# Performance work log

Measured on AMD Instinct MI355X. Metric: run time of the kernel, lower is better.

The kernel has to match this reference:

```python
import jax, jax.numpy as jnp
import numpy as np

B, LP, LE, D, H, DK, DV, DF = 16, 2047, 2048, 1024, 16, 64, 64, 4096


def _layer_norm(x, g, b, eps=1e-5):
    m = x.mean(-1, keepdims=True)
    v = ((x - m) ** 2).mean(-1, keepdims=True)
    return (x - m) * jax.lax.rsqrt(v + eps) * g + b


def _mha(q, kv, wq, wk, wv, wo, bo, g, b):
    # q: [B,Q,D], kv: [B,L,D]; per-head projections wq/wk: [H,D,DK], wv: [H,D,DV]
    residual = q
    Q = jnp.einsum('bqd,hdk->bhqk', q, wq)
    K = jnp.einsum('bld,hdk->bhlk', kv, wk)
    V = jnp.einsum('bld,hdv->bhlv', kv, wv)
    scale = jnp.sqrt(jnp.asarray(Q.shape[-1], Q.dtype))
    attn = jax.nn.softmax(jnp.einsum('bhqk,bhlk->bhql', Q, K) / scale, axis=-1)
    o = jnp.einsum('bhql,bhlv->bhqv', attn, V)
    o = o.transpose(0, 2, 1, 3).reshape(q.shape[0], q.shape[1], -1)  # concat heads
    o = o @ wo + bo
    return _layer_norm(o + residual, g, b), attn


def setup_inputs() -> dict:
    key = jax.random.key(0)
    ks = jax.random.split(key, 16)
    s = 0.02
    inp = {
        'dec_input': jax.random.normal(ks[0], (B, 1, D), jnp.float32),
        'input_history': jax.random.normal(ks[1], (B, LP, D), jnp.float32),
        'enc_output': jax.random.normal(ks[2], (B, LE, D), jnp.float32),
        'wq_s': jax.random.normal(ks[3], (H, D, DK), jnp.float32) * s,
        'wk_s': jax.random.normal(ks[4], (H, D, DK), jnp.float32) * s,
        'wv_s': jax.random.normal(ks[5], (H, D, DV), jnp.float32) * s,
        'wo_s': jax.random.normal(ks[6], (H * DV, D), jnp.float32) * s,
        'bo_s': jnp.zeros((D,), jnp.float32),
        'ln1_g': jnp.ones((D,), jnp.float32),
        'ln1_b': jnp.zeros((D,), jnp.float32),
        'wq_c': jax.random.normal(ks[7], (H, D, DK), jnp.float32) * s,
        'wk_c': jax.random.normal(ks[8], (H, D, DK), jnp.float32) * s,
        'wv_c': jax.random.normal(ks[9], (H, D, DV), jnp.float32) * s,
        'wo_c': jax.random.normal(ks[10], (H * DV, D), jnp.float32) * s,
        'bo_c': jnp.zeros((D,), jnp.float32),
        'ln2_g': jnp.ones((D,), jnp.float32),
        'ln2_b': jnp.zeros((D,), jnp.float32),
        'ffn_w1': jax.random.normal(ks[11], (D, DF), jnp.float32) * s,
        'ffn_b1': jnp.zeros((DF,), jnp.float32),
        'ffn_w2': jax.random.normal(ks[12], (DF, D), jnp.float32) * s,
        'ffn_b2': jnp.zeros((D,), jnp.float32),
        'ln3_g': jnp.ones((D,), jnp.float32),
        'ln3_b': jnp.zeros((D,), jnp.float32),
    }
    return inp


def reference(dec_input, input_history, enc_output,
              wq_s, wk_s, wv_s, wo_s, bo_s, ln1_g, ln1_b,
              wq_c, wk_c, wv_c, wo_c, bo_c, ln2_g, ln2_b,
              ffn_w1, ffn_b1, ffn_w2, ffn_b2, ln3_g, ln3_b):
    # KV-cache growth: history <- cat(history, dec_input)
    history = jnp.concatenate([input_history, dec_input], axis=1)  # [B, LP+1, D]
    x, slf_attn = _mha(dec_input, history, wq_s, wk_s, wv_s, wo_s, bo_s, ln1_g, ln1_b)
    x, enc_attn = _mha(x, enc_output, wq_c, wk_c, wv_c, wo_c, bo_c, ln2_g, ln2_b)
    y = jax.nn.relu(x @ ffn_w1 + ffn_b1) @ ffn_w2 + ffn_b2
    out = _layer_norm(y + x, ln3_g, ln3_b)
    return (out, slf_attn, enc_attn)
```

## Files before the change

### kernel.cpp

```cpp
#include <hip/hip_runtime.h>
#include <hip/hip_bf16.h>
#include <stdint.h>
#include <stddef.h>


#define DEV __device__ __forceinline__

typedef __attribute__((ext_vector_type(8))) short bf16x8;
typedef __attribute__((ext_vector_type(4))) short bf16x4;
typedef __attribute__((ext_vector_type(4))) float f32x4;

DEV unsigned short f2b(float f){
  union { __hip_bfloat16 h; unsigned short u; } cv;
  cv.h = __float2bfloat16(f);
  return cv.u;
}
DEV float b2f(unsigned short u){
  union { unsigned int i; float f; } cv;
  cv.i = ((unsigned int)u) << 16;
  return cv.f;
}
DEV f32x4 mfma16(bf16x8 a, bf16x8 b, f32x4 c){
  return __builtin_amdgcn_mfma_f32_16x16x32_bf16(a, b, c, 0, 0, 0);
}

__global__ __launch_bounds__(256) void g_qA(const float* __restrict__ src,
    const float* __restrict__ wq, float* __restrict__ Qpart){
  int ks = blockIdx.x, h = blockIdx.y;
  int k0b = ks*128;
  __shared__ unsigned short lt[2][64*40];
  int t = threadIdx.x, lane = t & 63, w = t >> 6;
  int k_loc = t >> 3, n_off = (t & 7)*8;
  const float* apf = src + (size_t)(lane & 15)*1024 + (lane >> 4)*8 + k0b;
  const float* Wb = wq + (size_t)h*65536;
  f32x4 acc = {0.f,0.f,0.f,0.f};
  float4 x0, x1;
  auto LD = [&](int c){
    const float* wp = Wb + (size_t)(k0b + c*32 + k_loc)*64 + n_off;
    x0 = *(const float4*)wp;
    x1 = *(const float4*)(wp + 4);
  };
  auto ST = [&](int buf){
    unsigned short* p = &lt[buf][0];
    p[(n_off+0)*40 + k_loc] = f2b(x0.x);
    p[(n_off+1)*40 + k_loc] = f2b(x0.y);
    p[(n_off+2)*40 + k_loc] = f2b(x0.z);
    p[(n_off+3)*40 + k_loc] = f2b(x0.w);
    p[(n_off+4)*40 + k_loc] = f2b(x1.x);
    p[(n_off+5)*40 + k_loc] = f2b(x1.y);
    p[(n_off+6)*40 + k_loc] = f2b(x1.z);
    p[(n_off+7)*40 + k_loc] = f2b(x1.w);
  };
  LD(0); ST(0);
  for(int c=0; c<4; ++c){
    if(c+1 < 4) LD(c+1);
    __syncthreads();
    float4 a0 = *(const float4*)(apf + c*32);
    float4 a1 = *(const float4*)(apf + c*32 + 4);
    bf16x8 af;
    af[0]=(short)f2b(a0.x); af[1]=(short)f2b(a0.y);
    af[2]=(short)f2b(a0.z); af[3]=(short)f2b(a0.w);
    af[4]=(short)f2b(a1.x); af[5]=(short)f2b(a1.y);
    af[6]=(short)f2b(a1.z); af[7]=(short)f2b(a1.w);
    bf16x8 bv = *(const bf16x8*)&lt[c&1][(w*16 + (lane & 15))*40 + (lane >> 4)*8];
    acc = mfma16(af, bv, acc);
    if(c+1 < 4) ST((c+1)&1);
  }
  int col = w*16 + (lane & 15);
  int r0 = (lane >> 4)*4;
  #pragma unroll
  for(int i=0;i<4;++i)
    Qpart[ ((size_t)(h*8 + ks)*16 + r0 + i)*64 + col ] = acc[i];
}

__global__ __launch_bounds__(256) void g_qB(const float* __restrict__ wk,
    const float* __restrict__ Qpart, unsigned short* __restrict__ qpb){
  int dt = blockIdx.x, h = blockIdx.y;
  int t = threadIdx.x;
  __shared__ float Qs[1024];
  #pragma unroll
  for(int i=0;i<4;++i){
    int idx = i*256 + t;
    float s = 0.f;
    #pragma unroll
    for(int ks=0; ks<8; ++ks)
      s += Qpart[((size_t)h<<13) + (ks<<10) + idx];
    Qs[idx] = s * 0.125f;
  }
  __syncthreads();
  int d_loc = t & 63, bg = t >> 6;
  const float* wr = wk + (size_t)h*65536 + (size_t)(dt*64 + d_loc)*64;
  float acc[4] = {0.f,0.f,0.f,0.f};
  #pragma unroll
  for(int k4=0; k4<16; ++k4){
    float4 w4 = *(const float4*)(wr + k4*4);
    #pragma unroll
    for(int i=0;i<4;++i){
      const float* q = &Qs[(bg*4+i)*64 + k4*4];
      acc[i] += w4.x*q[0] + w4.y*q[1] + w4.z*q[2] + w4.w*q[3];
    }
  }
  #pragma unroll
  for(int i=0;i<4;++i)
    qpb[ ((size_t)(bg*4+i)*16 + h)*1024 + dt*64 + d_loc ] = f2b(acc[i]);
}

__global__ __launch_bounds__(256) void g_attn(const float* __restrict__ kvsrc,
    const float* __restrict__ decrow, const unsigned short* __restrict__ qpb,
    float* __restrict__ scr, unsigned short* __restrict__ partb,
    float* __restrict__ msum, int lsrc){
  int u = blockIdx.x, ns = u & 63, b = u >> 6;
  int t = threadIdx.x, lane = t & 63, w = t >> 6;
  int r = lane & 15, hi = lane >> 4;
  int slice0 = ns*32;

  __shared__ unsigned short lt[1024*20];
  __shared__ float red[1024];
  __shared__ unsigned short p_lds[16*40];
  __shared__ float f_lds[16];

  float4 ld[16];
  auto ISSUE = [&](int c){
    int row = slice0 + c*16 + r;
    const float* rpp = (row < lsrc) ? kvsrc + ((size_t)b*lsrc + row)*1024
                                    : decrow + (size_t)b*1024;
    rpp += w*256 + hi*8;
    #pragma unroll
    for(int kk=0; kk<8; ++kk){
      ld[kk*2+0] = *(const float4*)(rpp + kk*32);
      ld[kk*2+1] = *(const float4*)(rpp + kk*32 + 4);
    }
  };

  ISSUE(0);
  for(int i=t; i<16*40; i+=256) p_lds[i] = 0;

  bf16x8 qf[8];
  {
    const unsigned short* qp = qpb + ((size_t)b*16 + r)*1024 + w*256 + hi*8;
    #pragma unroll
    for(int kk=0;kk<8;++kk) qf[kk] = *(const bf16x8*)(qp + kk*32);
  }

  f32x4 acc[16];
  #pragma unroll
  for(int i=0;i<16;++i) acc[i] = (f32x4){0.f,0.f,0.f,0.f};
  float m_run = -1e30f, s_run = 0.f;

  __syncthreads();
  for(int c=0; c<2; ++c){
    f32x4 s_acc = {0.f,0.f,0.f,0.f};
    int colw = r ^ ((hi & 1) << 3);
    #pragma unroll
    for(int kk=0; kk<8; ++kk){
      float4 a0 = ld[kk*2], a1 = ld[kk*2+1];
      bf16x8 v;
      v[0]=(short)f2b(a0.x); v[1]=(short)f2b(a0.y);
      v[2]=(short)f2b(a0.z); v[3]=(short)f2b(a0.w);
      v[4]=(short)f2b(a1.x); v[5]=(short)f2b(a1.y);
      v[6]=(short)f2b(a1.z); v[7]=(short)f2b(a1.w);
      unsigned short* pt = &lt[(w*256 + hi*8 + kk*32)*20 + colw];
      #pragma unroll
      for(int j=0;j<8;++j) pt[j*20] = (unsigned short)v[j];
      s_acc = mfma16(v, qf[kk], s_acc);
    }
    if(c < 1) ISSUE(c+1);
    *(f32x4*)&red[t*4] = s_acc;
    __syncthreads();

    f32x4 ss = *(const f32x4*)&red[(0*64+lane)*4];
    ss += *(const f32x4*)&red[(1*64+lane)*4];
    ss += *(const f32x4*)&red[(2*64+lane)*4];
    ss += *(const f32x4*)&red[(3*64+lane)*4];
    float sf[4] = {ss[0], ss[1], ss[2], ss[3]};
    float mc = fmaxf(fmaxf(sf[0],sf[1]), fmaxf(sf[2],sf[3]));
    mc = fmaxf(mc, __shfl_xor(mc, 16));
    mc = fmaxf(mc, __shfl_xor(mc, 32));
    float nm = fmaxf(m_run, mc);
    float fch = __expf(m_run - nm);
    float pvv[4]; float ps = 0.f;
    #pragma unroll
    for(int i=0;i<4;++i){ pvv[i] = __expf(sf[i]-nm); ps += pvv[i]; }
    ps += __shfl_xor(ps, 16);
    ps += __shfl_xor(ps, 32);
    s_run = s_run*fch + ps;
    m_run = nm;
    if(w == 0){
      #pragma unroll
      for(int i=0;i<4;++i) p_lds[r*40 + hi*4 + i] = f2b(pvv[i]);
      if(hi == 0) f_lds[r] = fch;
      float* sp = scr + ((size_t)b*16 + r)*2048 + slice0 + c*16 + hi*4;
      *(float4*)sp = (float4){sf[0], sf[1], sf[2], sf[3]};
    }
    __syncthreads();

    f32x4 fv = *(const f32x4*)&f_lds[hi*4];
    bf16x8 pa = *(const bf16x8*)&p_lds[r*40 + hi*8];
    #pragma unroll
    for(int dc=0; dc<16; ++dc){
      acc[dc] *= fv;
      int d = w*256 + dc*16 + r;
      int col0 = (((hi & 1) ^ ((r >> 3) & 1)) << 3);
      bf16x4 blo = *(const bf16x4*)&lt[d*20 + col0];
      bf16x4 bhi = *(const bf16x4*)&lt[d*20 + col0 + 4];
      bf16x8 bv;
      bv[0]=blo[0]; bv[1]=blo[1]; bv[2]=blo[2]; bv[3]=blo[3];
      bv[4]=bhi[0]; bv[5]=bhi[1]; bv[6]=bhi[2]; bv[7]=bhi[3];
      acc[dc] = mfma16(pa, bv, acc[dc]);
    }
    __syncthreads();
  }
  unsigned short* pl = lt;
  #pragma unroll
  for(int dc=0; dc<16; ++dc)
    #pragma unroll
    for(int i=0;i<4;++i)
      pl[(hi*4+i)*1024 + w*256 + dc*16 + r] = f2b(acc[dc][i]);
  __syncthreads();
  {
    const uint4* s4 = (const uint4*)pl;
    uint4* d4 = (uint4*)(partb + (((size_t)b*64 + ns)*16)*1024);
    #pragma unroll
    for(int j=0;j<8;++j) d4[t + j*256] = s4[t + j*256];
  }
  if(w==0 && hi==0){
    msum[(((size_t)b*64 + ns)*16 + r)*2 + 0] = m_run;
    msum[(((size_t)b*64 + ns)*16 + r)*2 + 1] = s_run;
  }
}

__global__ __launch_bounds__(256) void g_comb(const float* __restrict__ msum,
    const float* __restrict__ scr, const unsigned short* __restrict__ partb,
    float* __restrict__ attn_out, unsigned short* __restrict__ ctxb){
  int dq = blockIdx.x, bh = blockIdx.y, b = bh >> 4, h = bh & 15;
  int t = threadIdx.x;
  __shared__ float e_lds[64];
  __shared__ float Mi[2];
  if(t < 64){
    float2 ms = *(const float2*)&msum[(((size_t)b*64 + t)*16 + h)*2];
    float M = ms.x;
    #pragma unroll
    for(int o=1; o<64; o<<=1) M = fmaxf(M, __shfl_xor(M, o));
    float e = __expf(ms.x - M)*ms.y;
    float S = e;
    #pragma unroll
    for(int o=1; o<64; o<<=1) S += __shfl_xor(S, o);
    e_lds[t] = __expf(ms.x - M)/S;
    if(t == 0){ Mi[0] = M; Mi[1] = 1.f/S; }
  }
  __syncthreads();
  float M = Mi[0], inv = Mi[1];
  const float* sp = scr + (size_t)bh*2048 + dq*512;
  float* po = attn_out + (size_t)bh*2048 + dq*512;
  po[t]     = __expf(sp[t]     - M)*inv;
  po[t+256] = __expf(sp[t+256] - M)*inv;
  int d = dq*256 + t;
  const unsigned short* pb0 = partb + ((size_t)b*64*16 + h)*1024 + d;
  float acc = 0.f;
  #pragma unroll 8
  for(int ns=0; ns<64; ++ns)
    acc += e_lds[ns]*b2f(pb0[(size_t)ns*16384]);
  ctxb[(size_t)bh*1024 + d] = f2b(acc);
}

__global__ __launch_bounds__(256) void g_vproj(const float* __restrict__ wv,
    const unsigned short* __restrict__ ctxb, float* __restrict__ opart){
  int ks = blockIdx.x, h = blockIdx.y;
  int k0b = ks*128;
  __shared__ unsigned short lt[2][64*40];
  int t = threadIdx.x, lane = t & 63, w = t >> 6;
  int k_loc = t >> 3, n_off = (t & 7)*8;
  const unsigned short* apb = ctxb + (size_t)(lane & 15)*16384 + (size_t)h*1024
                              + (lane >> 4)*8 + k0b;
  const float* Wb = wv + (size_t)h*65536;
  f32x4 acc = {0.f,0.f,0.f,0.f};
  float4 x0, x1;
  auto LD = [&](int c){
    const float* wp = Wb + (size_t)(k0b + c*32 + k_loc)*64 + n_off;
    x0 = *(const float4*)wp;
    x1 = *(const float4*)(wp + 4);
  };
  auto ST = [&](int buf){
    unsigned short* p = &lt[buf][0];
    p[(n_off+0)*40 + k_loc] = f2b(x0.x);
    p[(n_off+1)*40 + k_loc] = f2b(x0.y);
    p[(n_off+2)*40 + k_loc] = f2b(x0.z);
    p[(n_off+3)*40 + k_loc] = f2b(x0.w);
    p[(n_off+4)*40 + k_loc] = f2b(x1.x);
    p[(n_off+5)*40 + k_loc] = f2b(x1.y);
    p[(n_off+6)*40 + k_loc] = f2b(x1.z);
    p[(n_off+7)*40 + k_loc] = f2b(x1.w);
  };
  LD(0); ST(0);
  for(int c=0; c<4; ++c){
    if(c+1 < 4) LD(c+1);
    __syncthreads();
    bf16x8 af = *(const bf16x8*)(apb + c*32);
    bf16x8 bv = *(const bf16x8*)&lt[c&1][(w*16 + (lane & 15))*40 + (lane >> 4)*8];
    acc = mfma16(af, bv, acc);
    if(c+1 < 4) ST((c+1)&1);
  }
  int col = w*16 + (lane & 15);
  int r0 = (lane >> 4)*4;
  #pragma unroll
  for(int i=0;i<4;++i)
    opart[ ((size_t)(h*8 + ks)*16 + r0 + i)*64 + col ] = acc[i];
}

__global__ __launch_bounds__(256) void g_ovred(const float* __restrict__ opart,
    unsigned short* __restrict__ ob){
  int i = blockIdx.x*256 + threadIdx.x;
  int b = i >> 10, hv = i & 1023, h = hv >> 6, v = hv & 63;
  float s = 0.f;
  #pragma unroll
  for(int ks=0; ks<8; ++ks)
    s += opart[ ((size_t)(h*8 + ks)*16 + b)*64 + v ];
  ob[(size_t)b*1024 + hv] = f2b(s);
}

__global__ __launch_bounds__(256) void g_ln(const float* __restrict__ parts, int KS,
    const float* __restrict__ bias, const float* __restrict__ resid,
    const float* __restrict__ g, const float* __restrict__ bb,
    float* __restrict__ xout, unsigned short* __restrict__ xb16){
  int b = blockIdx.x, t = threadIdx.x;
  __shared__ float red[256];
  const float4* bias4  = (const float4*)bias;
  const float4* resid4 = (const float4*)resid + (size_t)b*256;
  const float4* parts4 = (const float4*)parts;
  float4 s = bias4[t];
  { float4 rr = resid4[t]; s.x+=rr.x; s.y+=rr.y; s.z+=rr.z; s.w+=rr.w; }
  #pragma unroll 4
  for(int k=0;k<KS;++k){
    float4 pp = parts4[((size_t)k*16 + b)*256 + t];
    s.x+=pp.x; s.y+=pp.y; s.z+=pp.z; s.w+=pp.w;
  }
  red[t] = s.x+s.y+s.z+s.w; __syncthreads();
  for(int off=128; off>0; off>>=1){ if(t<off) red[t]+=red[t+off]; __syncthreads(); }
  float mean = red[0]*(1.f/1024.f); __syncthreads();
  float dx=s.x-mean, dy=s.y-mean, dz=s.z-mean, dw=s.w-mean;
  red[t] = dx*dx+dy*dy+dz*dz+dw*dw; __syncthreads();
  for(int off=128; off>0; off>>=1){ if(t<off) red[t]+=red[t+off]; __syncthreads(); }
  float rstd = rsqrtf(red[0]*(1.f/1024.f) + 1e-5f);
  float4 g4 = ((const float4*)g)[t], b4 = ((const float4*)bb)[t];
  float4 y;
  y.x = dx*rstd*g4.x + b4.x;
  y.y = dy*rstd*g4.y + b4.y;
  y.z = dz*rstd*g4.z + b4.z;
  y.w = dw*rstd*g4.w + b4.w;
  if(xout) ((float4*)xout)[(size_t)b*256 + t] = y;
  if(xb16){
    ushort4 uu;
    uu.x = f2b(y.x); uu.y = f2b(y.y); uu.z = f2b(y.z); uu.w = f2b(y.w);
    ((ushort4*)xb16)[(size_t)b*256 + t] = uu;
  }
}

__global__ __launch_bounds__(256) void g_skg(const float* __restrict__ W,
    const unsigned short* __restrict__ A, float* __restrict__ part,
    int N, int K, int KS){
  int nt = blockIdx.x, ks = blockIdx.y;
  int Ksl = K / KS, k0b = ks * Ksl, n0 = nt*64;
  int nc = Ksl >> 5;
  __shared__ unsigned short lt[2][64*40];
  int t = threadIdx.x, lane = t & 63, w = t >> 6;
  int k_loc = t >> 3, n_off = (t & 7)*8;
  const unsigned short* apb = A + (size_t)(lane & 15)*K + (lane >> 4)*8 + k0b;
  f32x4 acc = {0.f,0.f,0.f,0.f};
  float4 x0, x1;
  auto LD = [&](int c){
    const float* wp = W + (size_t)(k0b + c*32 + k_loc)*N + n0 + n_off;
    x0 = *(const float4*)wp;
    x1 = *(const float4*)(wp + 4);
  };
  auto ST = [&](int buf){
    unsigned short* p = &lt[buf][0];
    p[(n_off+0)*40 + k_loc] = f2b(x0.x);
    p[(n_off+1)*40 + k_loc] = f2b(x0.y);
    p[(n_off+2)*40 + k_loc] = f2b(x0.z);
    p[(n_off+3)*40 + k_loc] = f2b(x0.w);
    p[(n_off+4)*40 + k_loc] = f2b(x1.x);
    p[(n_off+5)*40 + k_loc] = f2b(x1.y);
    p[(n_off+6)*40 + k_loc] = f2b(x1.z);
    p[(n_off+7)*40 + k_loc] = f2b(x1.w);
  };
  LD(0); ST(0);
  for(int c=0; c<nc; ++c){
    if(c+1 < nc) LD(c+1);
    __syncthreads();
    bf16x8 af = *(const bf16x8*)(apb + c*32);
    bf16x8 bv = *(const bf16x8*)&lt[c&1][(w*16 + (lane & 15))*40 + (lane >> 4)*8];
    acc = mfma16(af, bv, acc);
    if(c+1 < nc) ST((c+1)&1);
  }
  int col = n0 + w*16 + (lane & 15);
  int r0 = (lane >> 4)*4;
  #pragma unroll
  for(int i=0;i<4;++i)
    part[ ((size_t)ks*16 + r0 + i)*(size_t)N + col ] = acc[i];
}

__global__ __launch_bounds__(256) void g_relu(const float* __restrict__ parts, int KS,
    const float* __restrict__ b1, unsigned short* __restrict__ h1){
  int i = blockIdx.x*256 + threadIdx.x;
  int b = i >> 10, f4 = i & 1023;
  float4 s = ((const float4*)b1)[f4];
  #pragma unroll 4
  for(int k=0;k<KS;++k){
    float4 pp = ((const float4*)parts)[((size_t)k*16 + b)*1024 + f4];
    s.x+=pp.x; s.y+=pp.y; s.z+=pp.z; s.w+=pp.w;
  }
  ushort4 uu;
  uu.x = f2b(fmaxf(s.x,0.f)); uu.y = f2b(fmaxf(s.y,0.f));
  uu.z = f2b(fmaxf(s.z,0.f)); uu.w = f2b(fmaxf(s.w,0.f));
  ((ushort4*)h1)[i] = uu;
}

extern "C" void kernel_launch(void* const* d_in, const int* in_sizes, int n_in,
                              void* d_out, int out_size, void* d_ws, size_t ws_size,
                              hipStream_t stream){
  const float* dec    = (const float*)d_in[0];
  const float* hist   = (const float*)d_in[1];
  const float* enc    = (const float*)d_in[2];
  const float* wq_s   = (const float*)d_in[3];
  const float* wk_s   = (const float*)d_in[4];
  const float* wv_s   = (const float*)d_in[5];
  const float* wo_s   = (const float*)d_in[6];
  const float* bo_s   = (const float*)d_in[7];
  const float* ln1_g  = (const float*)d_in[8];
  const float* ln1_b  = (const float*)d_in[9];
  const float* wq_c   = (const float*)d_in[10];
  const float* wk_c   = (const float*)d_in[11];
  const float* wv_c   = (const float*)d_in[12];
  const float* wo_c   = (const float*)d_in[13];
  const float* bo_c   = (const float*)d_in[14];
  const float* ln2_g  = (const float*)d_in[15];
  const float* ln2_b  = (const float*)d_in[16];
  const float* w1     = (const float*)d_in[17];
  const float* b1     = (const float*)d_in[18];
  const float* w2     = (const float*)d_in[19];
  const float* b2     = (const float*)d_in[20];
  const float* ln3_g  = (const float*)d_in[21];
  const float* ln3_b  = (const float*)d_in[22];

  float* out  = (float*)d_out;
  float* slf  = out + 16384;
  float* enco = out + 16384 + 524288;

  char* w = (char*)d_ws;
  float*          scr    = (float*)(w + 0x0000000);
  unsigned short* partb  = (unsigned short*)(w + 0x0200000);
  float*          msum   = (float*)(w + 0x2200000);
  unsigned short* qpb    = (unsigned short*)(w + 0x2240000);
  unsigned short* ctxb   = (unsigned short*)(w + 0x22C0000);
  float*          Qpart  = (float*)(w + 0x2340000);
  float*          opart  = (float*)(w + 0x23C0000);
  unsigned short* ob     = (unsigned short*)(w + 0x2440000);
  float*          x1     = (float*)(w + 0x2450000);
  float*          x2     = (float*)(w + 0x2460000);
  unsigned short* x2b    = (unsigned short*)(w + 0x2470000);
  unsigned short* h1b    = (unsigned short*)(w + 0x2480000);
  float*          gpart  = (float*)(w + 0x2500000);
  float*          fpart  = (float*)(w + 0x2600000);
  float*          g2part = (float*)(w + 0x2800000);

  g_qA   <<<dim3(8,16),  256, 0, stream>>>(dec, wq_s, Qpart);
  g_qB   <<<dim3(16,16), 256, 0, stream>>>(wk_s, Qpart, qpb);
  g_attn <<<1024, 256, 0, stream>>>(hist, dec, qpb, scr, partb, msum, 2047);
  g_comb <<<dim3(4,256), 256, 0, stream>>>(msum, scr, partb, slf, ctxb);
  g_vproj<<<dim3(8,16),  256, 0, stream>>>(wv_s, ctxb, opart);
  g_ovred<<<64,   256, 0, stream>>>(opart, ob);
  g_skg  <<<dim3(16,16), 256, 0, stream>>>(wo_s, ob, gpart, 1024, 1024, 16);
  g_ln   <<<16,   256, 0, stream>>>(gpart, 16, bo_s, dec, ln1_g, ln1_b, x1, (unsigned short*)0);

  g_qA   <<<dim3(8,16),  256, 0, stream>>>(x1, wq_c, Qpart);
  g_qB   <<<dim3(16,16), 256, 0, stream>>>(wk_c, Qpart, qpb);
  g_attn <<<1024, 256, 0, stream>>>(enc, dec, qpb, scr, partb, msum, 2048);
  g_comb <<<dim3(4,256), 256, 0, stream>>>(msum, scr, partb, enco, ctxb);
  g_vproj<<<dim3(8,16),  256, 0, stream>>>(wv_c, ctxb, opart);
  g_ovred<<<64,   256, 0, stream>>>(opart, ob);
  g_skg  <<<dim3(16,16), 256, 0, stream>>>(wo_c, ob, gpart, 1024, 1024, 16);
  g_ln   <<<16,   256, 0, stream>>>(gpart, 16, bo_c, x1, ln2_g, ln2_b, x2, x2b);

  g_skg  <<<dim3(64,8),  256, 0, stream>>>(w1, x2b, fpart, 4096, 1024, 8);
  g_relu <<<64,  256, 0, stream>>>(fpart, 8, b1, h1b);
  g_skg  <<<dim3(16,32), 256, 0, stream>>>(w2, h1b, g2part, 1024, 4096, 32);
  g_ln   <<<16,  256, 0, stream>>>(g2part, 32, b2, x2, ln3_g, ln3_b, out, (unsigned short*)0);
}
```

Measured before the change: 166.8 us.

## Fuse Q/K projection, V/O projection and ReLU reduction into fewer kernels

Merges the split-K Q projection and its reduction with the Wk query-folding into one kernel, so the Q partial buffer and one launch go away. It also fuses the V projection, its reduction and the Wo projection into one per-head kernel that writes per-head partials for the layer norm. The ReLU and bias reduction is folded into the A-operand load of the second FFN GEMM. Launch count and intermediate traffic drop, but each fused kernel now recomputes the full-K Q and V projections per block with fewer blocks (4x16), so parallelism falls and work is duplicated.

```diff
diff --git a/kernel.cpp b/kernel.cpp
--- a/kernel.cpp
+++ b/kernel.cpp
@@ -24,19 +24,20 @@
   return __builtin_amdgcn_mfma_f32_16x16x32_bf16(a, b, c, 0, 0, 0);
 }
 
-__global__ __launch_bounds__(256) void g_qA(const float* __restrict__ src,
-    const float* __restrict__ wq, float* __restrict__ Qpart){
-  int ks = blockIdx.x, h = blockIdx.y;
-  int k0b = ks*128;
+__global__ __launch_bounds__(256) void g_qp(const float* __restrict__ src,
+    const float* __restrict__ wq, const float* __restrict__ wk,
+    unsigned short* __restrict__ qpb){
+  int dt = blockIdx.x, h = blockIdx.y;
   __shared__ unsigned short lt[2][64*40];
+  __shared__ float Qs[1024];
   int t = threadIdx.x, lane = t & 63, w = t >> 6;
   int k_loc = t >> 3, n_off = (t & 7)*8;
-  const float* apf = src + (size_t)(lane & 15)*1024 + (lane >> 4)*8 + k0b;
+  const float* apf = src + (size_t)(lane & 15)*1024 + (lane >> 4)*8;
   const float* Wb = wq + (size_t)h*65536;
   f32x4 acc = {0.f,0.f,0.f,0.f};
   float4 x0, x1;
   auto LD = [&](int c){
-    const float* wp = Wb + (size_t)(k0b + c*32 + k_loc)*64 + n_off;
+    const float* wp = Wb + (size_t)(c*32 + k_loc)*64 + n_off;
     x0 = *(const float4*)wp;
     x1 = *(const float4*)(wp + 4);
   };
@@ -52,8 +53,8 @@
     p[(n_off+7)*40 + k_loc] = f2b(x1.w);
   };
   LD(0); ST(0);
-  for(int c=0; c<4; ++c){
-    if(c+1 < 4) LD(c+1);
+  for(int c=0; c<32; ++c){
+    if(c+1 < 32) LD(c+1);
     __syncthreads();
     float4 a0 = *(const float4*)(apf + c*32);
     float4 a1 = *(const float4*)(apf + c*32 + 4);
@@ -64,45 +65,32 @@
     af[6]=(short)f2b(a1.z); af[7]=(short)f2b(a1.w);
     bf16x8 bv = *(const bf16x8*)&lt[c&1][(w*16 + (lane & 15))*40 + (lane >> 4)*8];
     acc = mfma16(af, bv, acc);
-    if(c+1 < 4) ST((c+1)&1);
-  }
-  int col = w*16 + (lane & 15);
-  int r0 = (lane >> 4)*4;
-  #pragma unroll
-  for(int i=0;i<4;++i)
-    Qpart[ ((size_t)(h*8 + ks)*16 + r0 + i)*64 + col ] = acc[i];
-}
-
-__global__ __launch_bounds__(256) void g_qB(const float* __restrict__ wk,
-    const float* __restrict__ Qpart, unsigned short* __restrict__ qpb){
-  int dt = blockIdx.x, h = blockIdx.y;
-  int t = threadIdx.x;
-  __shared__ float Qs[1024];
-  #pragma unroll
-  for(int i=0;i<4;++i){
-    int idx = i*256 + t;
-    float s = 0.f;
-    #pragma unroll
-    for(int ks=0; ks<8; ++ks)
-      s += Qpart[((size_t)h<<13) + (ks<<10) + idx];
-    Qs[idx] = s * 0.125f;
+    if(c+1 < 32) ST((c+1)&1);
+  }
+  {
+    int col = w*16 + (lane & 15);
+    int r0 = (lane >> 4)*4;
+    #pragma unroll
+    for(int i=0;i<4;++i) Qs[(r0+i)*64 + col] = acc[i]*0.125f;
   }
   __syncthreads();
-  int d_loc = t & 63, bg = t >> 6;
-  const float* wr = wk + (size_t)h*65536 + (size_t)(dt*64 + d_loc)*64;
-  float acc[4] = {0.f,0.f,0.f,0.f};
+  int d = dt*256 + t;
+  const float* wr = wk + (size_t)h*65536 + (size_t)d*64;
+  float a16[16];
+  #pragma unroll
+  for(int b=0;b<16;++b) a16[b] = 0.f;
   #pragma unroll
   for(int k4=0; k4<16; ++k4){
     float4 w4 = *(const float4*)(wr + k4*4);
     #pragma unroll
-    for(int i=0;i<4;++i){
-      const float* q = &Qs[(bg*4+i)*64 + k4*4];
-      acc[i] += w4.x*q[0] + w4.y*q[1] + w4.z*q[2] + w4.w*q[3];
+    for(int b=0;b<16;++b){
+      const float* q = &Qs[b*64 + k4*4];
+      a16[b] += w4.x*q[0] + w4.y*q[1] + w4.z*q[2] + w4.w*q[3];
     }
   }
   #pragma unroll
-  for(int i=0;i<4;++i)
-    qpb[ ((size_t)(bg*4+i)*16 + h)*1024 + dt*64 + d_loc ] = f2b(acc[i]);
+  for(int b=0;b<16;++b)
+    qpb[((size_t)b*16 + h)*1024 + d] = f2b(a16[b]);
 }
 
 __global__ __launch_bounds__(256) void g_attn(const float* __restrict__ kvsrc,
@@ -263,20 +251,21 @@
   ctxb[(size_t)bh*1024 + d] = f2b(acc);
 }
 
-__global__ __launch_bounds__(256) void g_vproj(const float* __restrict__ wv,
-    const unsigned short* __restrict__ ctxb, float* __restrict__ opart){
-  int ks = blockIdx.x, h = blockIdx.y;
-  int k0b = ks*128;
+__global__ __launch_bounds__(256) void g_vwo(const float* __restrict__ wv,
+    const unsigned short* __restrict__ ctxb, const float* __restrict__ wo,
+    float* __restrict__ gpart){
+  int nt = blockIdx.x, h = blockIdx.y;
   __shared__ unsigned short lt[2][64*40];
+  __shared__ float obs[1024];
   int t = threadIdx.x, lane = t & 63, w = t >> 6;
   int k_loc = t >> 3, n_off = (t & 7)*8;
   const unsigned short* apb = ctxb + (size_t)(lane & 15)*16384 + (size_t)h*1024
-                              + (lane >> 4)*8 + k0b;
+                              + (lane >> 4)*8;
   const float* Wb = wv + (size_t)h*65536;
   f32x4 acc = {0.f,0.f,0.f,0.f};
   float4 x0, x1;
   auto LD = [&](int c){
-    const float* wp = Wb + (size_t)(k0b + c*32 + k_loc)*64 + n_off;
+    const float* wp = Wb + (size_t)(c*32 + k_loc)*64 + n_off;
     x0 = *(const float4*)wp;
     x1 = *(const float4*)(wp + 4);
   };
@@ -292,30 +281,34 @@
     p[(n_off+7)*40 + k_loc] = f2b(x1.w);
   };
   LD(0); ST(0);
-  for(int c=0; c<4; ++c){
-    if(c+1 < 4) LD(c+1);
+  for(int c=0; c<32; ++c){
+    if(c+1 < 32) LD(c+1);
     __syncthreads();
     bf16x8 af = *(const bf16x8*)(apb + c*32);
     bf16x8 bv = *(const bf16x8*)&lt[c&1][(w*16 + (lane & 15))*40 + (lane >> 4)*8];
     acc = mfma16(af, bv, acc);
-    if(c+1 < 4) ST((c+1)&1);
-  }
-  int col = w*16 + (lane & 15);
-  int r0 = (lane >> 4)*4;
-  #pragma unroll
-  for(int i=0;i<4;++i)
-    opart[ ((size_t)(h*8 + ks)*16 + r0 + i)*64 + col ] = acc[i];
-}
-
-__global__ __launch_bounds__(256) void g_ovred(const float* __restrict__ opart,
-    unsigned short* __restrict__ ob){
-  int i = blockIdx.x*256 + threadIdx.x;
-  int b = i >> 10, hv = i & 1023, h = hv >> 6, v = hv & 63;
-  float s = 0.f;
-  #pragma unroll
-  for(int ks=0; ks<8; ++ks)
-    s += opart[ ((size_t)(h*8 + ks)*16 + b)*64 + v ];
-  ob[(size_t)b*1024 + hv] = f2b(s);
+    if(c+1 < 32) ST((c+1)&1);
+  }
+  {
+    int col = w*16 + (lane & 15);
+    int r0 = (lane >> 4)*4;
+    #pragma unroll
+    for(int i=0;i<4;++i) obs[(r0+i)*64 + col] = acc[i];
+  }
+  __syncthreads();
+  int n = nt*256 + t;
+  const float* wrow = wo + (size_t)(h*64)*1024 + n;
+  float a16[16];
+  #pragma unroll
+  for(int b=0;b<16;++b) a16[b] = 0.f;
+  for(int v=0; v<64; ++v){
+    float wv_ = wrow[(size_t)v*1024];
+    #pragma unroll
+    for(int b=0;b<16;++b) a16[b] += obs[b*64 + v]*wv_;
+  }
+  #pragma unroll
+  for(int b=0;b<16;++b)
+    gpart[((size_t)h*16 + b)*1024 + n] = a16[b];
 }
 
 __global__ __launch_bounds__(256) void g_ln(const float* __restrict__ parts, int KS,
@@ -399,20 +392,64 @@
     part[ ((size_t)ks*16 + r0 + i)*(size_t)N + col ] = acc[i];
 }
 
-__global__ __launch_bounds__(256) void g_relu(const float* __restrict__ parts, int KS,
-    const float* __restrict__ b1, unsigned short* __restrict__ h1){
-  int i = blockIdx.x*256 + threadIdx.x;
-  int b = i >> 10, f4 = i & 1023;
-  float4 s = ((const float4*)b1)[f4];
-  #pragma unroll 4
-  for(int k=0;k<KS;++k){
-    float4 pp = ((const float4*)parts)[((size_t)k*16 + b)*1024 + f4];
-    s.x+=pp.x; s.y+=pp.y; s.z+=pp.z; s.w+=pp.w;
-  }
-  ushort4 uu;
-  uu.x = f2b(fmaxf(s.x,0.f)); uu.y = f2b(fmaxf(s.y,0.f));
-  uu.z = f2b(fmaxf(s.z,0.f)); uu.w = f2b(fmaxf(s.w,0.f));
-  ((ushort4*)h1)[i] = uu;
+__global__ __launch_bounds__(256) void g_skgf(const float* __restrict__ W,
+    const float* __restrict__ fpart, const float* __restrict__ b1,
+    float* __restrict__ part){
+  const int N = 1024, K = 4096, KS = 32;
+  int nt = blockIdx.x, ks = blockIdx.y;
+  int Ksl = K / KS, k0b = ks * Ksl, n0 = nt*64;
+  int nc = Ksl >> 5;
+  __shared__ unsigned short lt[2][64*40];
+  int t = threadIdx.x, lane = t & 63, w = t >> 6;
+  int k_loc = t >> 3, n_off = (t & 7)*8;
+  int arow = lane & 15, akof = (lane >> 4)*8;
+  f32x4 acc = {0.f,0.f,0.f,0.f};
+  float4 x0, x1;
+  auto LD = [&](int c){
+    const float* wp = W + (size_t)(k0b + c*32 + k_loc)*N + n0 + n_off;
+    x0 = *(const float4*)wp;
+    x1 = *(const float4*)(wp + 4);
+  };
+  auto ST = [&](int buf){
+    unsigned short* p = &lt[buf][0];
+    p[(n_off+0)*40 + k_loc] = f2b(x0.x);
+    p[(n_off+1)*40 + k_loc] = f2b(x0.y);
+    p[(n_off+2)*40 + k_loc] = f2b(x0.z);
+    p[(n_off+3)*40 + k_loc] = f2b(x0.w);
+    p[(n_off+4)*40 + k_loc] = f2b(x1.x);
+    p[(n_off+5)*40 + k_loc] = f2b(x1.y);
+    p[(n_off+6)*40 + k_loc] = f2b(x1.z);
+    p[(n_off+7)*40 + k_loc] = f2b(x1.w);
+  };
+  LD(0); ST(0);
+  for(int c=0; c<nc; ++c){
+    if(c+1 < nc) LD(c+1);
+    int kk = k0b + c*32 + akof;
+    float4 s0 = *(const float4*)(b1 + kk);
+    float4 s1 = *(const float4*)(b1 + kk + 4);
+    #pragma unroll
+    for(int p=0; p<8; ++p){
+      const float* fp = fpart + ((size_t)p*16 + arow)*4096 + kk;
+      float4 p0 = *(const float4*)fp;
+      float4 p1 = *(const float4*)(fp + 4);
+      s0.x+=p0.x; s0.y+=p0.y; s0.z+=p0.z; s0.w+=p0.w;
+      s1.x+=p1.x; s1.y+=p1.y; s1.z+=p1.z; s1.w+=p1.w;
+    }
+    bf16x8 af;
+    af[0]=(short)f2b(fmaxf(s0.x,0.f)); af[1]=(short)f2b(fmaxf(s0.y,0.f));
+    af[2]=(short)f2b(fmaxf(s0.z,0.f)); af[3]=(short)f2b(fmaxf(s0.w,0.f));
+    af[4]=(short)f2b(fmaxf(s1.x,0.f)); af[5]=(short)f2b(fmaxf(s1.y,0.f));
+    af[6]=(short)f2b(fmaxf(s1.z,0.f)); af[7]=(short)f2b(fmaxf(s1.w,0.f));
+    __syncthreads();
+    bf16x8 bv = *(const bf16x8*)&lt[c&1][(w*16 + (lane & 15))*40 + (lane >> 4)*8];
+    acc = mfma16(af, bv, acc);
+    if(c+1 < nc) ST((c+1)&1);
+  }
+  int col = n0 + w*16 + (lane & 15);
+  int r0 = (lane >> 4)*4;
+  #pragma unroll
+  for(int i=0;i<4;++i)
+    part[ ((size_t)ks*16 + r0 + i)*(size_t)N + col ] = acc[i];
 }
 
 extern "C" void kernel_launch(void* const* d_in, const int* in_sizes, int n_in,
@@ -452,37 +489,26 @@
   float*          msum   = (float*)(w + 0x2200000);
   unsigned short* qpb    = (unsigned short*)(w + 0x2240000);
   unsigned short* ctxb   = (unsigned short*)(w + 0x22C0000);
-  float*          Qpart  = (float*)(w + 0x2340000);
-  float*          opart  = (float*)(w + 0x23C0000);
-  unsigned short* ob     = (unsigned short*)(w + 0x2440000);
   float*          x1     = (float*)(w + 0x2450000);
   float*          x2     = (float*)(w + 0x2460000);
   unsigned short* x2b    = (unsigned short*)(w + 0x2470000);
-  unsigned short* h1b    = (unsigned short*)(w + 0x2480000);
   float*          gpart  = (float*)(w + 0x2500000);
   float*          fpart  = (float*)(w + 0x2600000);
   float*          g2part = (float*)(w + 0x2800000);
 
-  g_qA   <<<dim3(8,16),  256, 0, stream>>>(dec, wq_s, Qpart);
-  g_qB   <<<dim3(16,16), 256, 0, stream>>>(wk_s, Qpart, qpb);
+  g_qp   <<<dim3(4,16),  256, 0, stream>>>(dec, wq_s, wk_s, qpb);
   g_attn <<<1024, 256, 0, stream>>>(hist, dec, qpb, scr, partb, msum, 2047);
   g_comb <<<dim3(4,256), 256, 0, stream>>>(msum, scr, partb, slf, ctxb);
-  g_vproj<<<dim3(8,16),  256, 0, stream>>>(wv_s, ctxb, opart);
-  g_ovred<<<64,   256, 0, stream>>>(opart, ob);
-  g_skg  <<<dim3(16,16), 256, 0, stream>>>(wo_s, ob, gpart, 1024, 1024, 16);
+  g_vwo  <<<dim3(4,16),  256, 0, stream>>>(wv_s, ctxb, wo_s, gpart);
   g_ln   <<<16,   256, 0, stream>>>(gpart, 16, bo_s, dec, ln1_g, ln1_b, x1, (unsigned short*)0);
 
-  g_qA   <<<dim3(8,16),  256, 0, stream>>>(x1, wq_c, Qpart);
-  g_qB   <<<dim3(16,16), 256, 0, stream>>>(wk_c, Qpart, qpb);
+  g_qp   <<<dim3(4,16),  256, 0, stream>>>(x1, wq_c, wk_c, qpb);
   g_attn <<<1024, 256, 0, stream>>>(enc, dec, qpb, scr, partb, msum, 2048);
   g_comb <<<dim3(4,256), 256, 0, stream>>>(msum, scr, partb, enco, ctxb);
-  g_vproj<<<dim3(8,16),  256, 0, stream>>>(wv_c, ctxb, opart);
-  g_ovred<<<64,   256, 0, stream>>>(opart, ob);
-  g_skg  <<<dim3(16,16), 256, 0, stream>>>(wo_c, ob, gpart, 1024, 1024, 16);
+  g_vwo  <<<dim3(4,16),  256, 0, stream>>>(wv_c, ctxb, wo_c, gpart);
   g_ln   <<<16,   256, 0, stream>>>(gpart, 16, bo_c, x1, ln2_g, ln2_b, x2, x2b);
 
   g_skg  <<<dim3(64,8),  256, 0, stream>>>(w1, x2b, fpart, 4096, 1024, 8);
-  g_relu <<<64,  256, 0, stream>>>(fpart, 8, b1, h1b);
-  g_skg  <<<dim3(16,32), 256, 0, stream>>>(w2, h1b, g2part, 1024, 4096, 32);
+  g_skgf <<<dim3(16,32), 256, 0, stream>>>(w2, fpart, b1, g2part);
   g_ln   <<<16,  256, 0, stream>>>(g2part, 32, b2, x2, ln3_g, ln3_b, out, (unsigned short*)0);
 }
```

Result: slower. 251.4 us (+50.7%).
